# Kernel optimization log

Hardware: AMD Instinct MI355X
Metric: run time of the kernel (lower is better)

The kernel has to match this reference:

```python
import jax, jax.numpy as jnp
import numpy as np

N = 1500
GAT_IN = 32
GAT_OUT = 8
MLP_HIDDEN = 128
ALPHA = 0.2  # leaky relu slope
NEG_INF = -9.0e15


def setup_inputs() -> dict:
    key = jax.random.key(0)
    ks = jax.random.split(key, 16)
    eye = jnp.eye(N, dtype=jnp.float32)
    geo_adj = jnp.maximum((jax.random.uniform(ks[0], (N, N)) < 0.02).astype(jnp.float32), eye)
    sem_adj = jnp.maximum((jax.random.uniform(ks[1], (N, N)) < 0.02).astype(jnp.float32), eye)
    features = jax.random.normal(ks[2], (N, GAT_IN), dtype=jnp.float32)
    # all (i, j) region pairs, as in the original source
    ii, jj = jnp.meshgrid(jnp.arange(N), jnp.arange(N), indexing='ij')
    region_pairs = jnp.stack([ii.reshape(-1), jj.reshape(-1)], axis=1).astype(jnp.int64)
    distance_features = jax.random.uniform(ks[3], (N * N, 1), dtype=jnp.float32)
    def lin(k, fan_in, fan_out):
        return jax.random.normal(k, (fan_in, fan_out), dtype=jnp.float32) / jnp.sqrt(jnp.float32(fan_in))
    W0 = lin(ks[4], GAT_IN, GAT_OUT)
    W1 = lin(ks[5], GAT_OUT, GAT_OUT)
    W2 = lin(ks[6], GAT_OUT, GAT_OUT)
    a0 = lin(ks[7], 2 * GAT_OUT, 1)
    a1 = lin(ks[8], 2 * GAT_OUT, 1)
    a2 = lin(ks[9], 2 * GAT_OUT, 1)
    fc1_w = lin(ks[10], 2 * GAT_OUT + 1, MLP_HIDDEN)
    fc1_b = jnp.zeros((MLP_HIDDEN,), dtype=jnp.float32)
    fc2_w = lin(ks[11], MLP_HIDDEN, 1)
    fc2_b = jnp.zeros((1,), dtype=jnp.float32)
    return {"geo_adj": geo_adj, "sem_adj": sem_adj, "features": features,
            "region_pairs": region_pairs, "distance_features": distance_features,
            "W0": W0, "W1": W1, "W2": W2, "a0": a0, "a1": a1, "a2": a2,
            "fc1_w": fc1_w, "fc1_b": fc1_b, "fc2_w": fc2_w, "fc2_b": fc2_b}


def _gat_layer(combined_adj, feats, W, a):
    # h = W feats; attention score a([h_i || h_j]) decomposes into h_i@a1 + h_j@a2
    h = feats @ W                      # [N, out]
    f_src = h @ a[:GAT_OUT]            # [N, 1]
    f_dst = h @ a[GAT_OUT:]            # [N, 1]
    e = jax.nn.leaky_relu(f_src + f_dst.T, negative_slope=ALPHA)  # [N, N]
    e = e * combined_adj
    att = jax.nn.softmax(jnp.where(combined_adj > 0, e, NEG_INF), axis=1)
    return jax.nn.elu(att @ h)


def reference(geo_adj, sem_adj, features, region_pairs, distance_features,
              W0, W1, W2, a0, a1, a2, fc1_w, fc1_b, fc2_w, fc2_b):
    combined_adj = geo_adj + sem_adj
    enc = features
    for W, a in ((W0, a0), (W1, a1), (W2, a2)):
        enc = _gat_layer(combined_adj, enc, W, a)
    r1 = enc[region_pairs[:, 0]]       # [N^2, out]
    r2 = enc[region_pairs[:, 1]]       # [N^2, out]
    comb = jnp.concatenate([r1, r2, distance_features], axis=1)  # [N^2, 17]
    hid = jax.nn.relu(comb @ fc1_w + fc1_b)
    return hid @ fc2_w + fc2_b
```

## Files before the change

### kernel.cpp

```cpp
#include <hip/hip_runtime.h>
#include <hip/hip_bf16.h>

#define NN 1500
#define GIN 32
#define GOUT 8
#define HID 128
#define CAP 192

typedef float v2f __attribute__((ext_vector_type(2)));

__global__ void gat_first(const float* __restrict__ geo,
                          const float* __restrict__ sem,
                          const float* __restrict__ feat,
                          const float* __restrict__ W0,
                          const float* __restrict__ a0,
                          int* __restrict__ csr_idx,
                          float* __restrict__ csr_val,
                          int* __restrict__ csr_cnt,
                          float* __restrict__ enc_out) {
    const int i = blockIdx.x;
    const int t = threadIdx.x;
    __shared__ int cnt;
    __shared__ int sidx[CAP];
    __shared__ float sval[CAP];
    __shared__ float hi_s[GOUT];
    __shared__ float wsum[4][GOUT + 1];
    if (t == 0) cnt = 0;
    __syncthreads();

    const float* grow = geo + (size_t)i * NN;
    const float* srow = sem + (size_t)i * NN;
    for (int q = t; q < NN / 4; q += 256) {
        float4 g = *(const float4*)(grow + 4 * q);
        float4 s = *(const float4*)(srow + 4 * q);
        float a[4] = {g.x + s.x, g.y + s.y, g.z + s.z, g.w + s.w};
        #pragma unroll
        for (int c = 0; c < 4; ++c) {
            if (a[c] > 0.f) {
                int p = atomicAdd(&cnt, 1);
                if (p < CAP) { sidx[p] = 4 * q + c; sval[p] = a[c]; }
            }
        }
    }
    if (t < GOUT) {
        float hv = 0.f;
        #pragma unroll 4
        for (int c = 0; c < GIN; ++c)
            hv = fmaf(feat[(size_t)i * GIN + c], W0[c * GOUT + t], hv);
        hi_s[t] = hv;
    }
    __syncthreads();

    const int c2 = cnt < CAP ? cnt : CAP;
    if (t == 0) csr_cnt[i] = c2;
    for (int p = t; p < c2; p += 256) {
        csr_idx[(size_t)i * CAP + p] = sidx[p];
        csr_val[(size_t)i * CAP + p] = sval[p];
    }
    float fsrc = 0.f;
    #pragma unroll
    for (int k = 0; k < GOUT; ++k) fsrc = fmaf(hi_s[k], a0[k], fsrc);

    float den = 0.f;
    float num[GOUT] = {};
    if (t < c2) {
        int j = sidx[t];
        float a = sval[t];
        float hj[GOUT] = {};
        #pragma unroll
        for (int c4 = 0; c4 < GIN / 4; ++c4) {
            float4 e4 = *(const float4*)(feat + (size_t)j * GIN + 4 * c4);
            const float* ep = (const float*)&e4;
            #pragma unroll
            for (int c = 0; c < 4; ++c)
                #pragma unroll
                for (int k = 0; k < GOUT; ++k)
                    hj[k] = fmaf(ep[c], W0[(4 * c4 + c) * GOUT + k], hj[k]);
        }
        float fd = 0.f;
        #pragma unroll
        for (int k = 0; k < GOUT; ++k) fd = fmaf(hj[k], a0[GOUT + k], fd);
        float ev = fsrc + fd;
        ev = (ev > 0.f) ? ev : 0.2f * ev;
        ev *= a;
        float p = __expf(ev);
        den = p;
        #pragma unroll
        for (int k = 0; k < GOUT; ++k) num[k] = p * hj[k];
    }
    #pragma unroll
    for (int off = 32; off > 0; off >>= 1) {
        den += __shfl_xor(den, off, 64);
        #pragma unroll
        for (int k = 0; k < GOUT; ++k) num[k] += __shfl_xor(num[k], off, 64);
    }
    if ((t & 63) == 0) {
        wsum[t >> 6][0] = den;
        #pragma unroll
        for (int k = 0; k < GOUT; ++k) wsum[t >> 6][1 + k] = num[k];
    }
    __syncthreads();
    if (t < GOUT) {
        float L = wsum[0][0] + wsum[1][0] + wsum[2][0] + wsum[3][0];
        float v = (wsum[0][1 + t] + wsum[1][1 + t] + wsum[2][1 + t] + wsum[3][1 + t]) / L;
        enc_out[(size_t)i * GOUT + t] = (v > 0.f) ? v : (__expf(v) - 1.f);
    }
}

template<int IN>
__global__ void gat_layer(const float* __restrict__ enc,
                          const float* __restrict__ W,
                          const float* __restrict__ avec,
                          const int* __restrict__ csr_idx,
                          const float* __restrict__ csr_val,
                          const int* __restrict__ csr_cnt,
                          float* __restrict__ enc_out) {
    const int tid = threadIdx.x;
    const int lane = tid & 63;
    const int i = blockIdx.x * 4 + (tid >> 6);

    float hv = 0.f;
    if (lane < GOUT) {
        #pragma unroll 4
        for (int c = 0; c < IN; ++c)
            hv = fmaf(enc[(size_t)i * IN + c], W[c * GOUT + lane], hv);
    }
    float hi[GOUT];
    #pragma unroll
    for (int c = 0; c < GOUT; ++c) hi[c] = __shfl(hv, c, 64);
    float fsrc = 0.f;
    #pragma unroll
    for (int c = 0; c < GOUT; ++c) fsrc = fmaf(hi[c], avec[c], fsrc);

    const int cnt = csr_cnt[i];
    float den = 0.f;
    float num[GOUT] = {};
    for (int e = lane; e < cnt; e += 64) {
        int j = csr_idx[(size_t)i * CAP + e];
        float a = csr_val[(size_t)i * CAP + e];
        float hj[GOUT] = {};
        #pragma unroll
        for (int c4 = 0; c4 < IN / 4; ++c4) {
            float4 e4 = *(const float4*)(enc + (size_t)j * IN + 4 * c4);
            const float* ep = (const float*)&e4;
            #pragma unroll
            for (int c = 0; c < 4; ++c)
                #pragma unroll
                for (int k = 0; k < GOUT; ++k)
                    hj[k] = fmaf(ep[c], W[(4 * c4 + c) * GOUT + k], hj[k]);
        }
        float fd = 0.f;
        #pragma unroll
        for (int k = 0; k < GOUT; ++k) fd = fmaf(hj[k], avec[GOUT + k], fd);
        float ev = fsrc + fd;
        ev = (ev > 0.f) ? ev : 0.2f * ev;
        ev *= a;
        float p = __expf(ev);
        den += p;
        #pragma unroll
        for (int k = 0; k < GOUT; ++k) num[k] = fmaf(p, hj[k], num[k]);
    }
    #pragma unroll
    for (int off = 32; off > 0; off >>= 1) {
        den += __shfl_xor(den, off, 64);
        #pragma unroll
        for (int k = 0; k < GOUT; ++k) num[k] += __shfl_xor(num[k], off, 64);
    }
    if (lane < GOUT) {
        float v = num[lane] / den;
        enc_out[(size_t)i * GOUT + lane] = (v > 0.f) ? v : (__expf(v) - 1.f);
    }
}

#define MTI 96
#define MTJ 48
#define KS 64
#define KSTR 68

__global__ __launch_bounds__(256, 2) void mlp_kernel(
        const float* __restrict__ enc,
        const float* __restrict__ dist,
        const float* __restrict__ fc1w,
        const float* __restrict__ fc1b,
        const float* __restrict__ fc2w,
        const float* __restrict__ fc2b,
        float* __restrict__ out) {
    __shared__ float Us[MTI * KSTR];
    __shared__ float Vs[MTJ * KSTR];

    const int tid = threadIdx.x;
    const int i0 = blockIdx.y * MTI;
    const int j0 = blockIdx.x * MTJ;
    const int tx = tid & 15;
    const int ty = tid >> 4;

    const float* w16g = fc1w + 2 * GOUT * HID;

    int irow[6], jcol[3];
    float d[6][3];
    #pragma unroll
    for (int ii = 0; ii < 6; ++ii) irow[ii] = i0 + ty + 16 * ii;
    #pragma unroll
    for (int jj = 0; jj < 3; ++jj) jcol[jj] = j0 + tx + 16 * jj;
    #pragma unroll
    for (int ii = 0; ii < 6; ++ii) {
        int ic = irow[ii] < NN ? irow[ii] : NN - 1;
        #pragma unroll
        for (int jj = 0; jj < 3; ++jj) {
            int jc = jcol[jj] < NN ? jcol[jj] : NN - 1;
            d[ii][jj] = dist[(size_t)ic * NN + jc];
        }
    }

    v2f acc[6][3] = {};

    #pragma unroll
    for (int ph = 0; ph < 2; ++ph) {
        const int k0 = ph * KS;
        if (ph) __syncthreads();
        for (int u = tid; u < (MTI + MTJ) * 16; u += 256) {
            const int isU = (u < MTI * 16);
            const int q = isU ? u : u - MTI * 16;
            const int r = q >> 4;
            const int k4 = k0 + ((q & 15) << 2);
            int g = (isU ? i0 : j0) + r;
            if (g >= NN) g = NN - 1;
            float4 acc4;
            if (isU) acc4 = *(const float4*)(fc1b + k4);
            else acc4 = make_float4(0.f, 0.f, 0.f, 0.f);
            const float* wbase = fc1w + (isU ? 0 : GOUT) * HID + k4;
            const float* ep = enc + (size_t)g * GOUT;
            #pragma unroll
            for (int c = 0; c < GOUT; ++c) {
                float e = ep[c];
                float4 w4 = *(const float4*)(wbase + c * HID);
                acc4.x = fmaf(e, w4.x, acc4.x);
                acc4.y = fmaf(e, w4.y, acc4.y);
                acc4.z = fmaf(e, w4.z, acc4.z);
                acc4.w = fmaf(e, w4.w, acc4.w);
            }
            *(float4*)((isU ? Us : Vs) + r * KSTR + (k4 - k0)) = acc4;
        }
        __syncthreads();

        for (int k4 = 0; k4 < KS; k4 += 4) {
            float4 u4[6], v4[3];
            #pragma unroll
            for (int ii = 0; ii < 6; ++ii)
                u4[ii] = *(const float4*)(Us + (ty + 16 * ii) * KSTR + k4);
            #pragma unroll
            for (int jj = 0; jj < 3; ++jj)
                v4[jj] = *(const float4*)(Vs + (tx + 16 * jj) * KSTR + k4);
            v2f wlo = *(const v2f*)(w16g + k0 + k4);
            v2f whi = *(const v2f*)(w16g + k0 + k4 + 2);
            v2f flo = *(const v2f*)(fc2w + k0 + k4);
            v2f fhi = *(const v2f*)(fc2w + k0 + k4 + 2);
            #pragma unroll
            for (int h = 0; h < 2; ++h) {
                v2f w2 = h ? whi : wlo;
                v2f f2 = h ? fhi : flo;
                #pragma unroll
                for (int ii = 0; ii < 6; ++ii) {
                    v2f u2 = ((const v2f*)&u4[ii])[h];
                    #pragma unroll
                    for (int jj = 0; jj < 3; ++jj) {
                        v2f tt = u2 + ((const v2f*)&v4[jj])[h];
                        tt = __builtin_elementwise_fma((v2f)d[ii][jj], w2, tt);
                        tt = __builtin_elementwise_max(tt, (v2f)0.f);
                        acc[ii][jj] = __builtin_elementwise_fma(tt, f2, acc[ii][jj]);
                    }
                }
            }
        }
    }

    const float b2 = fc2b[0];
    #pragma unroll
    for (int ii = 0; ii < 6; ++ii) {
        if (irow[ii] >= NN) continue;
        #pragma unroll
        for (int jj = 0; jj < 3; ++jj) {
            if (jcol[jj] >= NN) continue;
            out[(size_t)irow[ii] * NN + jcol[jj]] = acc[ii][jj].x + acc[ii][jj].y + b2;
        }
    }
}

extern "C" void kernel_launch(void* const* d_in, const int* in_sizes, int n_in,
                              void* d_out, int out_size, void* d_ws, size_t ws_size,
                              hipStream_t stream) {
    const float* geo  = (const float*)d_in[0];
    const float* sem  = (const float*)d_in[1];
    const float* feat = (const float*)d_in[2];
    const float* dist = (const float*)d_in[4];
    const float* W0   = (const float*)d_in[5];
    const float* W1   = (const float*)d_in[6];
    const float* W2   = (const float*)d_in[7];
    const float* a0   = (const float*)d_in[8];
    const float* a1   = (const float*)d_in[9];
    const float* a2   = (const float*)d_in[10];
    const float* fc1w = (const float*)d_in[11];
    const float* fc1b = (const float*)d_in[12];
    const float* fc2w = (const float*)d_in[13];
    const float* fc2b = (const float*)d_in[14];
    float* out = (float*)d_out;

    char* ws = (char*)d_ws;
    int*   csr_idx = (int*)ws;                         ws += sizeof(int) * NN * CAP;
    float* csr_val = (float*)ws;                       ws += sizeof(float) * NN * CAP;
    int*   csr_cnt = (int*)ws;                         ws += sizeof(int) * NN;
    float* encA    = (float*)ws;                       ws += sizeof(float) * NN * GOUT;
    float* encB    = (float*)ws;

    gat_first<<<NN, 256, 0, stream>>>(geo, sem, feat, W0, a0,
                                      csr_idx, csr_val, csr_cnt, encA);
    gat_layer<GOUT><<<NN / 4, 256, 0, stream>>>(encA, W1, a1, csr_idx, csr_val, csr_cnt, encB);
    gat_layer<GOUT><<<NN / 4, 256, 0, stream>>>(encB, W2, a2, csr_idx, csr_val, csr_cnt, encA);

    dim3 mg(32, 16);
    mlp_kernel<<<mg, 256, 0, stream>>>(encA, dist, fc1w, fc1b, fc2w, fc2b, out);
}
```

Measured before the change: 160.2 us.

## Use relu identity and precompute U/V projections in last GAT layer

Rewrites relu(t) as (t+|t|)/2, so the linear part of the second MLP layer collapses into per-row and per-column scalars (Arow, Bcol, c) computed once. The inner loop then does one fma plus an abs-fma per k instead of add, fma, max and fma. The U/V hidden projections move into the final GAT layer kernel and are written to a workspace, so the MLP kernel only copies them into shared memory. MLP tiles become square 64x64 with 4x4 outputs per thread and launch_bounds raised to 4 blocks per CU. The cost is extra global traffic for the U/V buffers, and scalar code where the old version used packed v2f math.

```diff
diff --git a/kernel.cpp b/kernel.cpp
--- a/kernel.cpp
+++ b/kernel.cpp
@@ -6,8 +6,6 @@
 #define GOUT 8
 #define HID 128
 #define CAP 192
-
-typedef float v2f __attribute__((ext_vector_type(2)));
 
 __global__ void gat_first(const float* __restrict__ geo,
                           const float* __restrict__ sem,
@@ -107,14 +105,20 @@
     }
 }
 
-template<int IN>
+template<int IN, bool UV>
 __global__ void gat_layer(const float* __restrict__ enc,
                           const float* __restrict__ W,
                           const float* __restrict__ avec,
                           const int* __restrict__ csr_idx,
                           const float* __restrict__ csr_val,
                           const int* __restrict__ csr_cnt,
-                          float* __restrict__ enc_out) {
+                          float* __restrict__ enc_out,
+                          const float* __restrict__ fc1w,
+                          const float* __restrict__ fc1b,
+                          const float* __restrict__ fc2w,
+                          float* __restrict__ Ubuf, float* __restrict__ Vbuf,
+                          float* __restrict__ Arow, float* __restrict__ Bcol,
+                          float* __restrict__ cptr) {
     const int tid = threadIdx.x;
     const int lane = tid & 63;
     const int i = blockIdx.x * 4 + (tid >> 6);
@@ -166,122 +170,150 @@
         #pragma unroll
         for (int k = 0; k < GOUT; ++k) num[k] += __shfl_xor(num[k], off, 64);
     }
+    float vout = 0.f;
     if (lane < GOUT) {
         float v = num[lane] / den;
-        enc_out[(size_t)i * GOUT + lane] = (v > 0.f) ? v : (__expf(v) - 1.f);
+        vout = (v > 0.f) ? v : (__expf(v) - 1.f);
+        enc_out[(size_t)i * GOUT + lane] = vout;
+    }
+
+    if constexpr (UV) {
+        float er[GOUT];
+        #pragma unroll
+        for (int c = 0; c < GOUT; ++c) er[c] = __shfl(vout, c, 64);
+        const int kl = lane, kh = lane + 64;
+        float u_lo = fc1b[kl], u_hi = fc1b[kh];
+        float v_lo = 0.f, v_hi = 0.f;
+        #pragma unroll
+        for (int c = 0; c < GOUT; ++c) {
+            u_lo = fmaf(er[c], fc1w[c * HID + kl], u_lo);
+            u_hi = fmaf(er[c], fc1w[c * HID + kh], u_hi);
+            v_lo = fmaf(er[c], fc1w[(GOUT + c) * HID + kl], v_lo);
+            v_hi = fmaf(er[c], fc1w[(GOUT + c) * HID + kh], v_hi);
+        }
+        Ubuf[(size_t)i * HID + kl] = u_lo;
+        Ubuf[(size_t)i * HID + kh] = u_hi;
+        Vbuf[(size_t)i * HID + kl] = v_lo;
+        Vbuf[(size_t)i * HID + kh] = v_hi;
+        const float f_lo = fc2w[kl], f_hi = fc2w[kh];
+        float ap = u_lo * f_lo + u_hi * f_hi;
+        float bp = v_lo * f_lo + v_hi * f_hi;
+        #pragma unroll
+        for (int off = 32; off > 0; off >>= 1) {
+            ap += __shfl_xor(ap, off, 64);
+            bp += __shfl_xor(bp, off, 64);
+        }
+        if (lane == 0) { Arow[i] = ap; Bcol[i] = bp; }
+        if (i == 0) {
+            const float* w16g = fc1w + 2 * GOUT * HID;
+            float cp = w16g[kl] * f_lo + w16g[kh] * f_hi;
+            #pragma unroll
+            for (int off = 32; off > 0; off >>= 1) cp += __shfl_xor(cp, off, 64);
+            if (lane == 0) cptr[0] = cp;
+        }
     }
 }
 
-#define MTI 96
-#define MTJ 48
+#define BT 64
 #define KS 64
 #define KSTR 68
 
-__global__ __launch_bounds__(256, 2) void mlp_kernel(
-        const float* __restrict__ enc,
+__global__ __launch_bounds__(256, 4) void mlp_kernel(
+        const float* __restrict__ U, const float* __restrict__ V,
+        const float* __restrict__ Arow, const float* __restrict__ Bcol,
+        const float* __restrict__ cptr,
         const float* __restrict__ dist,
         const float* __restrict__ fc1w,
-        const float* __restrict__ fc1b,
         const float* __restrict__ fc2w,
         const float* __restrict__ fc2b,
         float* __restrict__ out) {
-    __shared__ float Us[MTI * KSTR];
-    __shared__ float Vs[MTJ * KSTR];
+    __shared__ float Us[BT * KSTR];
+    __shared__ float Vs[BT * KSTR];
 
     const int tid = threadIdx.x;
-    const int i0 = blockIdx.y * MTI;
-    const int j0 = blockIdx.x * MTJ;
+    const int i0 = blockIdx.y * BT;
+    const int j0 = blockIdx.x * BT;
     const int tx = tid & 15;
     const int ty = tid >> 4;
 
     const float* w16g = fc1w + 2 * GOUT * HID;
 
-    int irow[6], jcol[3];
-    float d[6][3];
-    #pragma unroll
-    for (int ii = 0; ii < 6; ++ii) irow[ii] = i0 + ty + 16 * ii;
-    #pragma unroll
-    for (int jj = 0; jj < 3; ++jj) jcol[jj] = j0 + tx + 16 * jj;
-    #pragma unroll
-    for (int ii = 0; ii < 6; ++ii) {
+    int irow[4], jcol[4];
+    float d[4][4];
+    #pragma unroll
+    for (int ii = 0; ii < 4; ++ii) irow[ii] = i0 + ty + 16 * ii;
+    #pragma unroll
+    for (int jj = 0; jj < 4; ++jj) jcol[jj] = j0 + tx + 16 * jj;
+    #pragma unroll
+    for (int ii = 0; ii < 4; ++ii) {
         int ic = irow[ii] < NN ? irow[ii] : NN - 1;
         #pragma unroll
-        for (int jj = 0; jj < 3; ++jj) {
+        for (int jj = 0; jj < 4; ++jj) {
             int jc = jcol[jj] < NN ? jcol[jj] : NN - 1;
             d[ii][jj] = dist[(size_t)ic * NN + jc];
         }
     }
 
-    v2f acc[6][3] = {};
+    float acc[4][4] = {};
 
     #pragma unroll
     for (int ph = 0; ph < 2; ++ph) {
         const int k0 = ph * KS;
         if (ph) __syncthreads();
-        for (int u = tid; u < (MTI + MTJ) * 16; u += 256) {
-            const int isU = (u < MTI * 16);
-            const int q = isU ? u : u - MTI * 16;
+        for (int u = tid; u < 2 * BT * 16; u += 256) {
+            const int isU = (u < BT * 16);
+            const int q = isU ? u : u - BT * 16;
             const int r = q >> 4;
-            const int k4 = k0 + ((q & 15) << 2);
+            const int kq = (q & 15) << 2;
             int g = (isU ? i0 : j0) + r;
             if (g >= NN) g = NN - 1;
-            float4 acc4;
-            if (isU) acc4 = *(const float4*)(fc1b + k4);
-            else acc4 = make_float4(0.f, 0.f, 0.f, 0.f);
-            const float* wbase = fc1w + (isU ? 0 : GOUT) * HID + k4;
-            const float* ep = enc + (size_t)g * GOUT;
-            #pragma unroll
-            for (int c = 0; c < GOUT; ++c) {
-                float e = ep[c];
-                float4 w4 = *(const float4*)(wbase + c * HID);
-                acc4.x = fmaf(e, w4.x, acc4.x);
-                acc4.y = fmaf(e, w4.y, acc4.y);
-                acc4.z = fmaf(e, w4.z, acc4.z);
-                acc4.w = fmaf(e, w4.w, acc4.w);
+            float4 val = *(const float4*)((isU ? U : V) + (size_t)g * HID + k0 + kq);
+            *(float4*)((isU ? Us : Vs) + r * KSTR + kq) = val;
+        }
+        __syncthreads();
+
+        #pragma unroll 2
+        for (int k4 = 0; k4 < KS; k4 += 4) {
+            float4 u4[4], v4[4];
+            #pragma unroll
+            for (int ii = 0; ii < 4; ++ii)
+                u4[ii] = *(const float4*)(Us + (ty + 16 * ii) * KSTR + k4);
+            #pragma unroll
+            for (int jj = 0; jj < 4; ++jj)
+                v4[jj] = *(const float4*)(Vs + (tx + 16 * jj) * KSTR + k4);
+            float wv[4], fv[4];
+            #pragma unroll
+            for (int kk = 0; kk < 4; ++kk) {
+                wv[kk] = w16g[k0 + k4 + kk];
+                fv[kk] = fc2w[k0 + k4 + kk];
             }
-            *(float4*)((isU ? Us : Vs) + r * KSTR + (k4 - k0)) = acc4;
-        }
-        __syncthreads();
-
-        for (int k4 = 0; k4 < KS; k4 += 4) {
-            float4 u4[6], v4[3];
-            #pragma unroll
-            for (int ii = 0; ii < 6; ++ii)
-                u4[ii] = *(const float4*)(Us + (ty + 16 * ii) * KSTR + k4);
-            #pragma unroll
-            for (int jj = 0; jj < 3; ++jj)
-                v4[jj] = *(const float4*)(Vs + (tx + 16 * jj) * KSTR + k4);
-            v2f wlo = *(const v2f*)(w16g + k0 + k4);
-            v2f whi = *(const v2f*)(w16g + k0 + k4 + 2);
-            v2f flo = *(const v2f*)(fc2w + k0 + k4);
-            v2f fhi = *(const v2f*)(fc2w + k0 + k4 + 2);
-            #pragma unroll
-            for (int h = 0; h < 2; ++h) {
-                v2f w2 = h ? whi : wlo;
-                v2f f2 = h ? fhi : flo;
+            #pragma unroll
+            for (int kk = 0; kk < 4; ++kk) {
                 #pragma unroll
-                for (int ii = 0; ii < 6; ++ii) {
-                    v2f u2 = ((const v2f*)&u4[ii])[h];
+                for (int ii = 0; ii < 4; ++ii) {
+                    float uk = ((const float*)&u4[ii])[kk];
                     #pragma unroll
-                    for (int jj = 0; jj < 3; ++jj) {
-                        v2f tt = u2 + ((const v2f*)&v4[jj])[h];
-                        tt = __builtin_elementwise_fma((v2f)d[ii][jj], w2, tt);
-                        tt = __builtin_elementwise_max(tt, (v2f)0.f);
-                        acc[ii][jj] = __builtin_elementwise_fma(tt, f2, acc[ii][jj]);
+                    for (int jj = 0; jj < 4; ++jj) {
+                        float t = fmaf(d[ii][jj], wv[kk],
+                                       uk + ((const float*)&v4[jj])[kk]);
+                        acc[ii][jj] = fmaf(fabsf(t), fv[kk], acc[ii][jj]);
                     }
                 }
             }
         }
     }
 
+    const float c = cptr[0];
     const float b2 = fc2b[0];
     #pragma unroll
-    for (int ii = 0; ii < 6; ++ii) {
+    for (int ii = 0; ii < 4; ++ii) {
         if (irow[ii] >= NN) continue;
-        #pragma unroll
-        for (int jj = 0; jj < 3; ++jj) {
+        const float Ai = Arow[irow[ii]];
+        #pragma unroll
+        for (int jj = 0; jj < 4; ++jj) {
             if (jcol[jj] >= NN) continue;
-            out[(size_t)irow[ii] * NN + jcol[jj]] = acc[ii][jj].x + acc[ii][jj].y + b2;
+            float lin = Ai + Bcol[jcol[jj]] + d[ii][jj] * c;
+            out[(size_t)irow[ii] * NN + jcol[jj]] = fmaf(0.5f, lin + acc[ii][jj], b2);
         }
     }
 }
@@ -310,13 +342,23 @@
     float* csr_val = (float*)ws;                       ws += sizeof(float) * NN * CAP;
     int*   csr_cnt = (int*)ws;                         ws += sizeof(int) * NN;
     float* encA    = (float*)ws;                       ws += sizeof(float) * NN * GOUT;
-    float* encB    = (float*)ws;
+    float* encB    = (float*)ws;                       ws += sizeof(float) * NN * GOUT;
+    float* Ubuf    = (float*)ws;                       ws += sizeof(float) * NN * HID;
+    float* Vbuf    = (float*)ws;                       ws += sizeof(float) * NN * HID;
+    float* Ar      = (float*)ws;                       ws += sizeof(float) * NN;
+    float* Bc      = (float*)ws;                       ws += sizeof(float) * NN;
+    float* cptr    = (float*)ws;
 
     gat_first<<<NN, 256, 0, stream>>>(geo, sem, feat, W0, a0,
                                       csr_idx, csr_val, csr_cnt, encA);
-    gat_layer<GOUT><<<NN / 4, 256, 0, stream>>>(encA, W1, a1, csr_idx, csr_val, csr_cnt, encB);
-    gat_layer<GOUT><<<NN / 4, 256, 0, stream>>>(encB, W2, a2, csr_idx, csr_val, csr_cnt, encA);
-
-    dim3 mg(32, 16);
-    mlp_kernel<<<mg, 256, 0, stream>>>(encA, dist, fc1w, fc1b, fc2w, fc2b, out);
+    gat_layer<GOUT, false><<<NN / 4, 256, 0, stream>>>(
+        encA, W1, a1, csr_idx, csr_val, csr_cnt, encB,
+        nullptr, nullptr, nullptr, nullptr, nullptr, nullptr, nullptr, nullptr);
+    gat_layer<GOUT, true><<<NN / 4, 256, 0, stream>>>(
+        encB, W2, a2, csr_idx, csr_val, csr_cnt, encA,
+        fc1w, fc1b, fc2w, Ubuf, Vbuf, Ar, Bc, cptr);
+
+    dim3 mg((NN + BT - 1) / BT, (NN + BT - 1) / BT);
+    mlp_kernel<<<mg, 256, 0, stream>>>(Ubuf, Vbuf, Ar, Bc, cptr,
+                                       dist, fc1w, fc2w, fc2b, out);
 }
```

Result: slower. 169.6 us (+5.8%).
